# Kernel tuning notes

Hardware: AMD Instinct MI355X
Metric: run time of the kernel (lower is better)

## Reference

```python
import jax, jax.numpy as jnp
import numpy as np

N_NODES = 100000
N_EDGES = 1200000
IN_DIM, HIDDEN, OUT_DIM = 128, 64, 64


def setup_inputs() -> dict:
    key = jax.random.key(0)
    k1, k2, k3, k4 = jax.random.split(key, 4)
    x = jax.random.normal(k1, (N_NODES, IN_DIM), dtype=jnp.float32)
    edge_index = jax.random.randint(k2, (2, N_EDGES), 0, N_NODES, dtype=jnp.int64)
    # Glorot-style init for GCNConv linear weights (PyG uses glorot), zero bias.
    W1 = jax.random.normal(k3, (IN_DIM, HIDDEN), dtype=jnp.float32) * np.float32(np.sqrt(2.0 / (IN_DIM + HIDDEN)))
    b1 = jnp.zeros((HIDDEN,), dtype=jnp.float32)
    W2 = jax.random.normal(k4, (HIDDEN, OUT_DIM), dtype=jnp.float32) * np.float32(np.sqrt(2.0 / (HIDDEN + OUT_DIM)))
    b2 = jnp.zeros((OUT_DIM,), dtype=jnp.float32)
    return {"x": x, "edge_index": edge_index, "W1": W1, "b1": b1, "W2": W2, "b2": b2}


def _gcn_conv(h, src, dst, deg_inv_sqrt, W, b):
    # PyG GCNConv: out = scatter_add( norm * (h @ W)[src] -> dst ) + b
    n = h.shape[0]
    norm = deg_inv_sqrt[src] * deg_inv_sqrt[dst]            # [E+N]
    hw = h @ W                                              # [N, F_out]
    msg = hw[src] * norm[:, None]                           # [E+N, F_out] gather
    out = jnp.zeros((n, W.shape[1]), h.dtype).at[dst].add(msg)  # scatter-add
    return out + b


def reference(x, edge_index, W1, b1, W2, b2):
    n = x.shape[0]
    # Add self-loops (GCNConv default add_self_loops=True).
    loop = jnp.arange(n, dtype=edge_index.dtype)
    src = jnp.concatenate([edge_index[0], loop])  # source nodes
    dst = jnp.concatenate([edge_index[1], loop])  # target nodes (aggregation)
    # Symmetric normalization D^{-1/2} (A+I) D^{-1/2}; degree at targets.
    deg = jnp.zeros((n,), x.dtype).at[dst].add(jnp.ones((), x.dtype))
    deg_inv_sqrt = jnp.where(deg > 0, jax.lax.rsqrt(deg), 0.0)
    h = _gcn_conv(x, src, dst, deg_inv_sqrt, W1, b1)
    h = jax.nn.relu(h)
    h = _gcn_conv(h, src, dst, deg_inv_sqrt, W2, b2)
    h = jax.nn.relu(h)
    return h
```

## Files before the change

### kernel.cpp

```cpp
#include <hip/hip_runtime.h>
#include <hip/hip_fp16.h>
#include <cstdint>
#include <cstddef>

#define NN 100000
#define NE 1200000
#define NBKT 1563
#define CAP_B 1536
#define PBLK 256
#define PCHK ((NE + PBLK - 1) / PBLK)

typedef _Float16 f16x8 __attribute__((ext_vector_type(8)));
typedef float f32x4 __attribute__((ext_vector_type(4)));

__global__ void zero_kernel(int* __restrict__ cur, unsigned* __restrict__ ovfn) {
    int i = blockIdx.x * blockDim.x + threadIdx.x;
    if (i < NBKT) cur[i] = 0;
    if (i == NBKT) *ovfn = 0;
}

__global__ __launch_bounds__(1024) void partition_hier(
    const int* __restrict__ ei, int* __restrict__ cur,
    unsigned* __restrict__ recs, unsigned* __restrict__ ovfn,
    uint2* __restrict__ ovf, int E) {
    __shared__ int hist[NBKT];
    __shared__ int base[NBKT];
    const int tid = threadIdx.x;
    for (int i = tid; i < NBKT; i += 1024) hist[i] = 0;
    __syncthreads();
    const int lo = blockIdx.x * PCHK, hi = min(lo + PCHK, E);
    for (int e = lo + tid; e < hi; e += 1024)
        atomicAdd(&hist[ei[E + e] >> 6], 1);
    __syncthreads();
    for (int i = tid; i < NBKT; i += 1024) {
        int c = hist[i];
        base[i] = c ? atomicAdd(&cur[i], c) : 0;
        hist[i] = 0;
    }
    __syncthreads();
    for (int e = lo + tid; e < hi; e += 1024) {
        int d = ei[E + e];
        int s = ei[e];
        int b = d >> 6;
        int lp = atomicAdd(&hist[b], 1);
        int pos = base[b] + lp;
        if (pos < CAP_B)
            recs[(size_t)b * CAP_B + pos] = ((unsigned)s << 6) | (unsigned)(d & 63);
        else {
            unsigned o = atomicAdd(ovfn, 1);
            if (o < 4096) ovf[o] = make_uint2((unsigned)s, (unsigned)d);
        }
    }
}

__global__ __launch_bounds__(256) void sort_bucket(
    const int* __restrict__ cur, unsigned* __restrict__ recs,
    const unsigned* __restrict__ ovfn, const uint2* __restrict__ ovf,
    float* __restrict__ dis, int* __restrict__ offn, int n) {
    __shared__ unsigned raw[CAP_B], srt[CAP_B];
    __shared__ int cnt[64], pfx[64], woff[64];
    const int b = blockIdx.x, tid = threadIdx.x;
    if (tid < 64) cnt[tid] = 0;
    const int c = min(cur[b], CAP_B);
    unsigned* slab = recs + (size_t)b * CAP_B;
    for (int i = tid; i < c; i += 256) raw[i] = slab[i];
    __syncthreads();
    for (int i = tid; i < c; i += 256) atomicAdd(&cnt[raw[i] & 63], 1);
    __syncthreads();
    if (tid < 64) pfx[tid] = cnt[tid];
    __syncthreads();
    for (int s = 1; s < 64; s <<= 1) {
        int v = (tid < 64 && tid >= s) ? pfx[tid - s] : 0;
        __syncthreads();
        if (tid < 64) pfx[tid] += v;
        __syncthreads();
    }
    if (tid < 64) woff[tid] = pfx[tid] - cnt[tid];
    __syncthreads();
    for (int i = tid; i < c; i += 256) {
        unsigned k = raw[i];
        int p = atomicAdd(&woff[k & 63], 1);
        srt[p] = k >> 6;
    }
    __syncthreads();
    for (int i = tid; i < c; i += 256) slab[i] = srt[i];
    if (tid < 64) {
        int g = b * 64 + tid;
        if (g < n) {
            int cc = cnt[tid];
            unsigned no = *ovfn;
            for (unsigned i = 0; i < no; i++)
                if ((int)ovf[i].y == g) cc++;
            dis[g] = rsqrtf((float)cc + 1.0f);
            offn[g] = pfx[tid] - cnt[tid];
        }
    }
}

#define LD1(q) { float2 g01 = __half22float2(*(__half2*)&(q).x); \
                 float2 g23 = __half22float2(*(__half2*)&(q).y); \
                 a0 += g01.x; a1 += g01.y; a2 += g23.x; a3 += g23.y; }

template <bool HALF_OUT>
__global__ __launch_bounds__(256) void agg_bucket4(
    const int* __restrict__ cur, const unsigned* __restrict__ recs,
    const int* __restrict__ offn, const __half* __restrict__ hw,
    const float* __restrict__ dis, const float* __restrict__ bias,
    void* __restrict__ outv,
    const unsigned* __restrict__ ovfn, const uint2* __restrict__ ovf, int n) {
    __shared__ unsigned srec[CAP_B];
    __shared__ int soff[65];
    __shared__ float disD[64];
    const int b = blockIdx.x, tid = threadIdx.x;
    const int c = min(cur[b], CAP_B);
    const unsigned* slab = recs + (size_t)b * CAP_B;
    for (int i = tid; i < c; i += 256) srec[i] = slab[i];
    if (tid < 64) {
        int g = b * 64 + tid;
        disD[tid] = (g < n) ? dis[g] : 0.f;
        soff[tid] = (g < n) ? offn[g] : c;
    }
    if (tid == 0) soff[64] = c;
    __syncthreads();

    const uint2* hwq = (const uint2*)hw;
    const int slot = tid >> 4, sub = tid & 15;
    const unsigned no = *ovfn;
    const float4 bb = ((const float4*)bias)[sub];

    for (int j = 0; j < 4; j++) {
        int nl = slot * 4 + j;
        int g = b * 64 + nl;
        if (g >= n) break;
        uint2 qs = hwq[(size_t)g * 16 + sub];
        float a0 = 0.f, a1 = 0.f, a2 = 0.f, a3 = 0.f;
        LD1(qs);

        int e = soff[nl], end = soff[nl + 1];
        for (; e + 8 <= end; e += 8) {
            uint2 q0 = hwq[(size_t)srec[e + 0] * 16 + sub];
            uint2 q1 = hwq[(size_t)srec[e + 1] * 16 + sub];
            uint2 q2 = hwq[(size_t)srec[e + 2] * 16 + sub];
            uint2 q3 = hwq[(size_t)srec[e + 3] * 16 + sub];
            uint2 q4 = hwq[(size_t)srec[e + 4] * 16 + sub];
            uint2 q5 = hwq[(size_t)srec[e + 5] * 16 + sub];
            uint2 q6 = hwq[(size_t)srec[e + 6] * 16 + sub];
            uint2 q7 = hwq[(size_t)srec[e + 7] * 16 + sub];
            LD1(q0); LD1(q1); LD1(q2); LD1(q3);
            LD1(q4); LD1(q5); LD1(q6); LD1(q7);
        }
        for (; e + 4 <= end; e += 4) {
            uint2 q0 = hwq[(size_t)srec[e + 0] * 16 + sub];
            uint2 q1 = hwq[(size_t)srec[e + 1] * 16 + sub];
            uint2 q2 = hwq[(size_t)srec[e + 2] * 16 + sub];
            uint2 q3 = hwq[(size_t)srec[e + 3] * 16 + sub];
            LD1(q0); LD1(q1); LD1(q2); LD1(q3);
        }
        for (; e < end; e++) {
            uint2 q = hwq[(size_t)srec[e] * 16 + sub];
            LD1(q);
        }
        for (unsigned i = 0; i < no; i++) {
            uint2 o = ovf[i];
            if ((int)o.y == g) { uint2 q = hwq[(size_t)o.x * 16 + sub]; LD1(q); }
        }
        float di = disD[nl];
        float o0 = fmaf(di, a0, bb.x);
        float o1 = fmaf(di, a1, bb.y);
        float o2 = fmaf(di, a2, bb.z);
        float o3 = fmaf(di, a3, bb.w);
        o0 = o0 > 0.f ? o0 : 0.f;
        o1 = o1 > 0.f ? o1 : 0.f;
        o2 = o2 > 0.f ? o2 : 0.f;
        o3 = o3 > 0.f ? o3 : 0.f;
        if (HALF_OUT) {
            __half2 p01 = __floats2half2_rn(o0, o1);
            __half2 p23 = __floats2half2_rn(o2, o3);
            uint2 pk;
            pk.x = *(unsigned*)&p01;
            pk.y = *(unsigned*)&p23;
            ((uint2*)outv)[(size_t)g * 16 + sub] = pk;
        } else {
            float4 oo; oo.x = o0; oo.y = o1; oo.z = o2; oo.w = o3;
            ((float4*)outv)[(size_t)g * 16 + sub] = oo;
        }
    }
}

template <int K>
__global__ __launch_bounds__(256) void gemm_mfma(const float* __restrict__ A,
                                                 const float* __restrict__ W,
                                                 const float* __restrict__ dis,
                                                 __half* __restrict__ C, int n) {
    constexpr int KB = K / 32;
    __shared__ f16x8 sAf[4 * KB * 64];
    __shared__ f16x8 sWf[4 * KB * 64];
    __shared__ float sdis[64];
    const int tid = threadIdx.x;
    const int row0 = blockIdx.x * 64;

    if (tid < 64) {
        int rw = row0 + tid;
        sdis[tid] = (rw < n) ? dis[rw] : 0.f;
    }

    _Float16* sAh = (_Float16*)sAf;
    const float4* A4 = (const float4*)A;
#pragma unroll
    for (int it = 0; it < K / 16; ++it) {
        int f = it * 256 + tid;
        int row = f / (K / 4);
        int kq = f % (K / 4);
        int k0 = kq * 4;
        float4 a;
        if (row0 + row < n) a = A4[(size_t)(row0 + row) * (K / 4) + kq];
        else { a.x = 0.f; a.y = 0.f; a.z = 0.f; a.w = 0.f; }
        int rt = row >> 4;
        int kb = k0 >> 5;
        int lane = (row & 15) | (((k0 >> 3) & 3) << 4);
        int base = ((rt * KB + kb) * 64 + lane) * 8 + (k0 & 7);
        sAh[base + 0] = (_Float16)a.x;
        sAh[base + 1] = (_Float16)a.y;
        sAh[base + 2] = (_Float16)a.z;
        sAh[base + 3] = (_Float16)a.w;
    }
    _Float16* sWh = (_Float16*)sWf;
    {
        int nn = tid & 63;
        int ct = nn >> 4;
        int lbase = nn & 15;
        for (int k = tid >> 6; k < K; k += 4) {
            float w = W[(size_t)k * 64 + nn];
            int kb = k >> 5;
            int lane = lbase | (((k >> 3) & 3) << 4);
            sWh[((ct * KB + kb) * 64 + lane) * 8 + (k & 7)] = (_Float16)w;
        }
    }
    __syncthreads();

    const int wv = tid >> 6;
    const int lane = tid & 63;
    f32x4 acc[4];
#pragma unroll
    for (int rt = 0; rt < 4; ++rt) acc[rt] = (f32x4){0.f, 0.f, 0.f, 0.f};

#pragma unroll
    for (int kb = 0; kb < KB; ++kb) {
        f16x8 bf = sWf[(wv * KB + kb) * 64 + lane];
#pragma unroll
        for (int rt = 0; rt < 4; ++rt) {
            f16x8 af = sAf[(rt * KB + kb) * 64 + lane];
            acc[rt] = __builtin_amdgcn_mfma_f32_16x16x32_f16(af, bf, acc[rt], 0, 0, 0);
        }
    }

    int col = wv * 16 + (lane & 15);
    int rbase = (lane >> 4) * 4;
#pragma unroll
    for (int rt = 0; rt < 4; ++rt) {
#pragma unroll
        for (int r = 0; r < 4; ++r) {
            int row = row0 + rt * 16 + rbase + r;
            if (row < n)
                C[(size_t)row * 64 + col] = __float2half(acc[rt][r] * sdis[rt * 16 + rbase + r]);
        }
    }
}

__global__ __launch_bounds__(256) void gemm_mfma_h(const __half* __restrict__ A,
                                                   const float* __restrict__ W,
                                                   const float* __restrict__ dis,
                                                   __half* __restrict__ C, int n) {
    constexpr int K = 64, KB = 2;
    __shared__ f16x8 sAf[4 * KB * 64];
    __shared__ f16x8 sWf[4 * KB * 64];
    __shared__ float sdis[64];
    const int tid = threadIdx.x;
    const int row0 = blockIdx.x * 64;

    if (tid < 64) {
        int rw = row0 + tid;
        sdis[tid] = (rw < n) ? dis[rw] : 0.f;
    }

    _Float16* sAh = (_Float16*)sAf;
    const uint2* A2 = (const uint2*)A;
#pragma unroll
    for (int it = 0; it < 4; ++it) {
        int f = it * 256 + tid;
        int row = f >> 4;
        int kq = f & 15;
        int k0 = kq * 4;
        uint2 a;
        if (row0 + row < n) a = A2[(size_t)(row0 + row) * 16 + kq];
        else { a.x = 0u; a.y = 0u; }
        _Float16* ap = (_Float16*)&a;
        int rt = row >> 4;
        int kb = k0 >> 5;
        int lane = (row & 15) | (((k0 >> 3) & 3) << 4);
        int base = ((rt * KB + kb) * 64 + lane) * 8 + (k0 & 7);
        sAh[base + 0] = ap[0];
        sAh[base + 1] = ap[1];
        sAh[base + 2] = ap[2];
        sAh[base + 3] = ap[3];
    }
    _Float16* sWh = (_Float16*)sWf;
    {
        int nn = tid & 63;
        int ct = nn >> 4;
        int lbase = nn & 15;
        for (int k = tid >> 6; k < K; k += 4) {
            float w = W[(size_t)k * 64 + nn];
            int kb = k >> 5;
            int lane = lbase | (((k >> 3) & 3) << 4);
            sWh[((ct * 2 + kb) * 64 + lane) * 8 + (k & 7)] = (_Float16)w;
        }
    }
    __syncthreads();

    const int wv = tid >> 6;
    const int lane = tid & 63;
    f32x4 acc[4];
#pragma unroll
    for (int rt = 0; rt < 4; ++rt) acc[rt] = (f32x4){0.f, 0.f, 0.f, 0.f};

#pragma unroll
    for (int kb = 0; kb < KB; ++kb) {
        f16x8 bf = sWf[(wv * KB + kb) * 64 + lane];
#pragma unroll
        for (int rt = 0; rt < 4; ++rt) {
            f16x8 af = sAf[(rt * KB + kb) * 64 + lane];
            acc[rt] = __builtin_amdgcn_mfma_f32_16x16x32_f16(af, bf, acc[rt], 0, 0, 0);
        }
    }

    int col = wv * 16 + (lane & 15);
    int rbase = (lane >> 4) * 4;
#pragma unroll
    for (int rt = 0; rt < 4; ++rt) {
#pragma unroll
        for (int r = 0; r < 4; ++r) {
            int row = row0 + rt * 16 + rbase + r;
            if (row < n)
                C[(size_t)row * 64 + col] = __float2half(acc[rt][r] * sdis[rt * 16 + rbase + r]);
        }
    }
}

__global__ void fill_kernel(float* __restrict__ p, float v, int n) {
    int i = blockIdx.x * blockDim.x + threadIdx.x;
    if (i < n) p[i] = v;
}
__global__ void degree_kernel(const int* __restrict__ ei, float* __restrict__ deg, int E) {
    int stride = gridDim.x * blockDim.x;
    for (int e = blockIdx.x * blockDim.x + threadIdx.x; e < E; e += stride)
        atomicAdd(&deg[ei[E + e]], 1.0f);
}
__global__ void rsqrt_kernel(float* __restrict__ deg, int n) {
    int i = blockIdx.x * blockDim.x + threadIdx.x;
    if (i < n) deg[i] = rsqrtf(deg[i]);
}
template <int K>
__global__ __launch_bounds__(256) void gemm_tile(const float* __restrict__ A,
                                                 const float* __restrict__ W,
                                                 float* __restrict__ C, int n) {
    __shared__ float sA[64 * K];
    __shared__ float sW[K * 64];
    const int tid = threadIdx.x;
    const int row0 = blockIdx.x * 64;
    const int rows = min(64, n - row0);
    const float4* W4 = (const float4*)W;
    float4* sW4 = (float4*)sW;
    for (int i = tid; i < K * 16; i += 256) sW4[i] = W4[i];
    const float4* A4 = (const float4*)(A + (size_t)row0 * K);
    float4* sA4 = (float4*)sA;
    const int nElem = rows * (K / 4);
    for (int i = tid; i < nElem; i += 256) sA4[i] = A4[i];
    __syncthreads();
    const int col = tid & 63;
    const int ty  = tid >> 6;
    float acc[16];
#pragma unroll
    for (int r = 0; r < 16; r++) acc[r] = 0.f;
    for (int k = 0; k < K; k += 4) {
        float w0 = sW[(k + 0) * 64 + col];
        float w1 = sW[(k + 1) * 64 + col];
        float w2 = sW[(k + 2) * 64 + col];
        float w3 = sW[(k + 3) * 64 + col];
#pragma unroll
        for (int r = 0; r < 16; r++) {
            const float4 a = *(const float4*)&sA[(ty + 4 * r) * K + k];
            acc[r] = fmaf(a.x, w0, acc[r]);
            acc[r] = fmaf(a.y, w1, acc[r]);
            acc[r] = fmaf(a.z, w2, acc[r]);
            acc[r] = fmaf(a.w, w3, acc[r]);
        }
    }
#pragma unroll
    for (int r = 0; r < 16; r++) {
        int row = ty + 4 * r;
        if (row < rows) C[(size_t)(row0 + row) * 64 + col] = acc[r];
    }
}
__global__ void scatter_kernel(const int* __restrict__ ei, const float* __restrict__ hw,
                               const float* __restrict__ dis, float* __restrict__ agg, int E) {
    int gtid = blockIdx.x * blockDim.x + threadIdx.x;
    int wave = gtid >> 6, lane = threadIdx.x & 63;
    int nwaves = (gridDim.x * blockDim.x) >> 6;
    for (int e = wave; e < E; e += nwaves) {
        int s = ei[e], d = ei[E + e];
        float v = hw[(size_t)s * 64 + lane] * dis[s] * dis[d];
        atomicAdd(&agg[(size_t)d * 64 + lane], v);
    }
}
__global__ void finalize_kernel(float* __restrict__ agg, const float* __restrict__ hw,
                                const float* __restrict__ dis, const float* __restrict__ b, int n) {
    int i = blockIdx.x * blockDim.x + threadIdx.x;
    if (i < n * 64) {
        int node = i >> 6, col = i & 63;
        float di = dis[node];
        float v = agg[i] + hw[i] * di * di + b[col];
        agg[i] = v > 0.0f ? v : 0.0f;
    }
}

extern "C" void kernel_launch(void* const* d_in, const int* in_sizes, int n_in,
                              void* d_out, int out_size, void* d_ws, size_t ws_size,
                              hipStream_t stream) {
    const float* x  = (const float*)d_in[0];
    const int*   ei = (const int*)d_in[1];
    const float* W1 = (const float*)d_in[2];
    const float* b1 = (const float*)d_in[3];
    const float* W2 = (const float*)d_in[4];
    const float* b2 = (const float*)d_in[5];
    float* out = (float*)d_out;

    const int N = NN, E = NE;
    char* ws = (char*)d_ws;
    const int gemmGrid = (N + 63) / 64;

    if (ws_size >= 38200000u) {
        float*    dis  = (float*)ws;
        int*      cur  = (int*)(ws + (1u << 19));
        unsigned* ovfn = (unsigned*)(ws + 589824u);
        uint2*    ovf  = (uint2*)(ws + 593920u);
        int*      offn = (int*)(ws + 655360u);
        unsigned* recs = (unsigned*)(ws + 1572864u);
        __half*   hwa  = (__half*)(ws + 11534336u);
        __half*   hvb  = (__half*)(ws + 25165824u);

        zero_kernel<<<(NBKT + 256) / 256, 256, 0, stream>>>(cur, ovfn);
        partition_hier<<<PBLK, 1024, 0, stream>>>(ei, cur, recs, ovfn, ovf, E);
        sort_bucket<<<NBKT, 256, 0, stream>>>(cur, recs, ovfn, ovf, dis, offn, N);

        gemm_mfma<128><<<gemmGrid, 256, 0, stream>>>(x, W1, dis, hwa, N);
        agg_bucket4<true><<<NBKT, 256, 0, stream>>>(cur, recs, offn, hwa, dis, b1, hvb, ovfn, ovf, N);
        gemm_mfma_h<<<gemmGrid, 256, 0, stream>>>(hvb, W2, dis, hwa, N);
        agg_bucket4<false><<<NBKT, 256, 0, stream>>>(cur, recs, offn, hwa, dis, b2, out, ovfn, ovf, N);
    } else {
        float* dis  = (float*)ws;
        float* bufA = (float*)(ws + (1 << 19));
        const size_t featBytes = (size_t)N * 64 * sizeof(float);

        fill_kernel<<<(N + 255) / 256, 256, 0, stream>>>(dis, 1.0f, N);
        degree_kernel<<<2048, 256, 0, stream>>>(ei, dis, E);
        rsqrt_kernel<<<(N + 255) / 256, 256, 0, stream>>>(dis, N);

        gemm_tile<128><<<gemmGrid, 256, 0, stream>>>(x, W1, bufA, N);
        hipMemsetAsync(out, 0, featBytes, stream);
        scatter_kernel<<<2048, 256, 0, stream>>>(ei, bufA, dis, out, E);
        finalize_kernel<<<(N * 64 + 255) / 256, 256, 0, stream>>>(out, bufA, dis, b1, N);

        gemm_tile<64><<<gemmGrid, 256, 0, stream>>>(out, W2, bufA, N);
        hipMemsetAsync(out, 0, featBytes, stream);
        scatter_kernel<<<2048, 256, 0, stream>>>(ei, bufA, dis, out, E);
        finalize_kernel<<<(N * 64 + 255) / 256, 256, 0, stream>>>(out, bufA, dis, b2, N);
    }
}
```

Before: 118.3 us.

## Use per-wave histograms in bucket sort and widen aggregation to 512 threads

The bucket sort now keeps a separate 64-entry histogram per wavefront and builds per-wave write offsets, so fewer threads contend on the same LDS atomics. The aggregation kernel is relaunched with 512 threads per block, each 16-lane slot covering 2 nodes instead of 4. It also gains a 16-way unrolled gather loop to keep more loads in flight. The larger blocks and wider unroll raise register pressure and may limit occupancy, and per-wave counting makes the order of edges within a node depend on the wave split.

```diff
diff --git a/kernel.cpp b/kernel.cpp
--- a/kernel.cpp
+++ b/kernel.cpp
@@ -58,16 +58,27 @@
     const unsigned* __restrict__ ovfn, const uint2* __restrict__ ovf,
     float* __restrict__ dis, int* __restrict__ offn, int n) {
     __shared__ unsigned raw[CAP_B], srt[CAP_B];
-    __shared__ int cnt[64], pfx[64], woff[64];
+    __shared__ int cnt4[4][64];
+    __shared__ int wb[4][64];
+    __shared__ int cnt[64], pfx[64];
     const int b = blockIdx.x, tid = threadIdx.x;
-    if (tid < 64) cnt[tid] = 0;
+    const int wv = tid >> 6;
+    cnt4[wv][tid & 63] = 0;
     const int c = min(cur[b], CAP_B);
     unsigned* slab = recs + (size_t)b * CAP_B;
     for (int i = tid; i < c; i += 256) raw[i] = slab[i];
     __syncthreads();
-    for (int i = tid; i < c; i += 256) atomicAdd(&cnt[raw[i] & 63], 1);
-    __syncthreads();
-    if (tid < 64) pfx[tid] = cnt[tid];
+    for (int i = tid; i < c; i += 256) atomicAdd(&cnt4[wv][raw[i] & 63], 1);
+    __syncthreads();
+    if (tid < 64) {
+        int c0 = cnt4[0][tid], c1 = cnt4[1][tid], c2 = cnt4[2][tid], c3 = cnt4[3][tid];
+        cnt[tid] = c0 + c1 + c2 + c3;
+        cnt4[0][tid] = 0;
+        cnt4[1][tid] = c0;
+        cnt4[2][tid] = c0 + c1;
+        cnt4[3][tid] = c0 + c1 + c2;
+        pfx[tid] = cnt[tid];
+    }
     __syncthreads();
     for (int s = 1; s < 64; s <<= 1) {
         int v = (tid < 64 && tid >= s) ? pfx[tid - s] : 0;
@@ -75,11 +86,17 @@
         if (tid < 64) pfx[tid] += v;
         __syncthreads();
     }
-    if (tid < 64) woff[tid] = pfx[tid] - cnt[tid];
+    if (tid < 64) {
+        int start = pfx[tid] - cnt[tid];
+        wb[0][tid] = start + cnt4[0][tid];
+        wb[1][tid] = start + cnt4[1][tid];
+        wb[2][tid] = start + cnt4[2][tid];
+        wb[3][tid] = start + cnt4[3][tid];
+    }
     __syncthreads();
     for (int i = tid; i < c; i += 256) {
         unsigned k = raw[i];
-        int p = atomicAdd(&woff[k & 63], 1);
+        int p = atomicAdd(&wb[wv][k & 63], 1);
         srt[p] = k >> 6;
     }
     __syncthreads();
@@ -102,7 +119,7 @@
                  a0 += g01.x; a1 += g01.y; a2 += g23.x; a3 += g23.y; }
 
 template <bool HALF_OUT>
-__global__ __launch_bounds__(256) void agg_bucket4(
+__global__ __launch_bounds__(512) void agg_bucket5(
     const int* __restrict__ cur, const unsigned* __restrict__ recs,
     const int* __restrict__ offn, const __half* __restrict__ hw,
     const float* __restrict__ dis, const float* __restrict__ bias,
@@ -114,7 +131,7 @@
     const int b = blockIdx.x, tid = threadIdx.x;
     const int c = min(cur[b], CAP_B);
     const unsigned* slab = recs + (size_t)b * CAP_B;
-    for (int i = tid; i < c; i += 256) srec[i] = slab[i];
+    for (int i = tid; i < c; i += 512) srec[i] = slab[i];
     if (tid < 64) {
         int g = b * 64 + tid;
         disD[tid] = (g < n) ? dis[g] : 0.f;
@@ -128,8 +145,8 @@
     const unsigned no = *ovfn;
     const float4 bb = ((const float4*)bias)[sub];
 
-    for (int j = 0; j < 4; j++) {
-        int nl = slot * 4 + j;
+    for (int j = 0; j < 2; j++) {
+        int nl = slot * 2 + j;
         int g = b * 64 + nl;
         if (g >= n) break;
         uint2 qs = hwq[(size_t)g * 16 + sub];
@@ -137,17 +154,19 @@
         LD1(qs);
 
         int e = soff[nl], end = soff[nl + 1];
+        for (; e + 16 <= end; e += 16) {
+            uint2 q[16];
+#pragma unroll
+            for (int t = 0; t < 16; t++) q[t] = hwq[(size_t)srec[e + t] * 16 + sub];
+#pragma unroll
+            for (int t = 0; t < 16; t++) { LD1(q[t]); }
+        }
         for (; e + 8 <= end; e += 8) {
-            uint2 q0 = hwq[(size_t)srec[e + 0] * 16 + sub];
-            uint2 q1 = hwq[(size_t)srec[e + 1] * 16 + sub];
-            uint2 q2 = hwq[(size_t)srec[e + 2] * 16 + sub];
-            uint2 q3 = hwq[(size_t)srec[e + 3] * 16 + sub];
-            uint2 q4 = hwq[(size_t)srec[e + 4] * 16 + sub];
-            uint2 q5 = hwq[(size_t)srec[e + 5] * 16 + sub];
-            uint2 q6 = hwq[(size_t)srec[e + 6] * 16 + sub];
-            uint2 q7 = hwq[(size_t)srec[e + 7] * 16 + sub];
-            LD1(q0); LD1(q1); LD1(q2); LD1(q3);
-            LD1(q4); LD1(q5); LD1(q6); LD1(q7);
+            uint2 q[8];
+#pragma unroll
+            for (int t = 0; t < 8; t++) q[t] = hwq[(size_t)srec[e + t] * 16 + sub];
+#pragma unroll
+            for (int t = 0; t < 8; t++) { LD1(q[t]); }
         }
         for (; e + 4 <= end; e += 4) {
             uint2 q0 = hwq[(size_t)srec[e + 0] * 16 + sub];
@@ -454,9 +473,9 @@
         sort_bucket<<<NBKT, 256, 0, stream>>>(cur, recs, ovfn, ovf, dis, offn, N);
 
         gemm_mfma<128><<<gemmGrid, 256, 0, stream>>>(x, W1, dis, hwa, N);
-        agg_bucket4<true><<<NBKT, 256, 0, stream>>>(cur, recs, offn, hwa, dis, b1, hvb, ovfn, ovf, N);
+        agg_bucket5<true><<<NBKT, 512, 0, stream>>>(cur, recs, offn, hwa, dis, b1, hvb, ovfn, ovf, N);
         gemm_mfma_h<<<gemmGrid, 256, 0, stream>>>(hvb, W2, dis, hwa, N);
-        agg_bucket4<false><<<NBKT, 256, 0, stream>>>(cur, recs, offn, hwa, dis, b2, out, ovfn, ovf, N);
+        agg_bucket5<false><<<NBKT, 512, 0, stream>>>(cur, recs, offn, hwa, dis, b2, out, ovfn, ovf, N);
     } else {
         float* dis  = (float*)ws;
         float* bufA = (float*)(ws + (1 << 19));
```

New measurement: 123.7 us. +4.6%, slower.
